# Optimization experiments

Measured on AMD Instinct MI355X. Metric: run time of the kernel, lower is better.

The kernel has to match this reference:

```python
import jax, jax.numpy as jnp
import numpy as np

HIDDEN = 1280
NUM_HEADS = 20
HEAD_DIM = HIDDEN // NUM_HEADS
B, S = 2, 2048


def setup_inputs() -> dict:
    key = jax.random.key(0)
    k1, k2, k3, k4, k5 = jax.random.split(key, 5)
    scale_in = 1.0 / np.sqrt(HIDDEN)
    return {
        "x": jax.random.normal(k1, (B, S, HIDDEN), dtype=jnp.float32),
        "w_attn": jax.random.normal(k2, (HIDDEN, 3 * HIDDEN), dtype=jnp.float32) * scale_in,
        "b_attn": jax.random.normal(k3, (3 * HIDDEN,), dtype=jnp.float32) * 0.02,
        "w_proj": jax.random.normal(k4, (HIDDEN, HIDDEN), dtype=jnp.float32) * scale_in,
        "b_proj": jax.random.normal(k5, (HIDDEN,), dtype=jnp.float32) * 0.02,
    }


def reference(x, w_attn, b_attn, w_proj, b_proj):
    b, s, _ = x.shape
    scale = 1.0 / np.sqrt(HEAD_DIM)
    qkv = x @ w_attn + b_attn                      # [B,S,3H]
    q, k, v = jnp.split(qkv, 3, axis=-1)

    def heads(t):  # [B,S,H] -> [B,nh,S,hd]
        return t.reshape(b, s, NUM_HEADS, HEAD_DIM).transpose(0, 2, 1, 3)

    q, k, v = heads(q), heads(k), heads(v)
    attn = jnp.einsum("bhqd,bhkd->bhqk", q, k) * scale
    causal = jnp.tril(jnp.ones((s, s), dtype=bool))
    attn = jnp.where(causal, attn, jnp.float32(-jnp.inf))
    attn = jax.nn.softmax(attn, axis=-1)           # dropout = identity (eval)
    out = jnp.einsum("bhqk,bhkd->bhqd", attn, v)
    out = out.transpose(0, 2, 1, 3).reshape(b, s, HIDDEN)
    return out @ w_proj + b_proj
```

## Files before the change

kernel.cpp:

```cpp
#include <hip/hip_runtime.h>

typedef unsigned short u16;
typedef __attribute__((ext_vector_type(8))) short bf16x8;
typedef __attribute__((ext_vector_type(4))) float f32x4;
typedef __attribute__((ext_vector_type(4))) unsigned short u16x4;

#define MFMA16 __builtin_amdgcn_mfma_f32_16x16x32_bf16

__device__ __forceinline__ u16 f2bf(float f) {
  unsigned int u = __float_as_uint(f);
  u += 0x7fff + ((u >> 16) & 1);
  return (u16)(u >> 16);
}

__device__ __forceinline__ float vexp2(float x) {
  float r; asm("v_exp_f32 %0, %1" : "=v"(r) : "v"(x)); return r;
}

template<int CTRL>
__device__ __forceinline__ float dppf(float v) {
  return __int_as_float(__builtin_amdgcn_update_dpp(0, __float_as_int(v), CTRL, 0xF, 0xF, true));
}
__device__ __forceinline__ float rowmax16(float v) {
  v = fmaxf(v, dppf<0xB1>(v));
  v = fmaxf(v, dppf<0x4E>(v));
  v = fmaxf(v, dppf<0x141>(v));
  v = fmaxf(v, dppf<0x140>(v));
  return v;
}
__device__ __forceinline__ float rowsum16(float v) {
  v += dppf<0xB1>(v);
  v += dppf<0x4E>(v);
  v += dppf<0x141>(v);
  v += dppf<0x140>(v);
  return v;
}

__device__ __forceinline__ void gload_lds16(const void* g, void* l) {
  __builtin_amdgcn_global_load_lds((__attribute__((address_space(1))) void*)g,
                                   (__attribute__((address_space(3))) void*)l,
                                   16, 0, 0);
}

__global__ void k_cast(const float* __restrict__ src, u16* __restrict__ dst, int n4) {
  int i = blockIdx.x * 256 + threadIdx.x;
  if (i >= n4) return;
  const float4 v = reinterpret_cast<const float4*>(src)[i];
  u16x4 o = {f2bf(v.x), f2bf(v.y), f2bf(v.z), f2bf(v.w)};
  reinterpret_cast<u16x4*>(dst)[i] = o;
}

__global__ void k_transpose_cast(const float* __restrict__ src, u16* __restrict__ dst,
                                 int R, int C) {
  __shared__ float tile[64][65];
  const int t = threadIdx.x;
  const int c0 = blockIdx.x * 64, r0 = blockIdx.y * 64;
#pragma unroll
  for (int i = 0; i < 16; ++i) {
    int e = i * 256 + t;
    int r = e >> 6, c = e & 63;
    tile[r][c] = src[(size_t)(r0 + r) * C + (c0 + c)];
  }
  __syncthreads();
#pragma unroll
  for (int i = 0; i < 16; ++i) {
    int e = i * 256 + t;
    int r = e >> 6, c = e & 63;
    dst[(size_t)(c0 + r) * R + (r0 + c)] = f2bf(tile[c][r]);
  }
}

__global__ void k_transpose_v(const u16* __restrict__ v, u16* __restrict__ vt) {
  __shared__ unsigned int tile[64][65];
  const int t = threadIdx.x;
  const int sblk = blockIdx.x, bh = blockIdx.y;
  {
    const int sl = t >> 2, d0 = (t & 3) * 16;
    const u16* src = v + ((size_t)(bh * 2048 + sblk * 64 + sl) * 64 + d0);
    bf16x8 a = *(const bf16x8*)src;
    bf16x8 b = *(const bf16x8*)(src + 8);
#pragma unroll
    for (int i = 0; i < 8; ++i) {
      tile[sl][d0 + i] = (u16)a[i];
      tile[sl][d0 + 8 + i] = (u16)b[i];
    }
  }
  __syncthreads();
  {
    const int d = t >> 2, s0 = (t & 3) * 16;
    bf16x8 o0, o1;
#pragma unroll
    for (int i = 0; i < 8; ++i) {
      o0[i] = (short)(u16)tile[s0 + i][d];
      o1[i] = (short)(u16)tile[s0 + 8 + i][d];
    }
    u16* dst = vt + ((size_t)(bh * 64 + d) * 2048 + sblk * 64 + s0);
    *(bf16x8*)dst = o0;
    *(bf16x8*)(dst + 8) = o1;
  }
}

__global__ __launch_bounds__(256, 2) void k_gemm_qkv(
    const u16* __restrict__ A, const u16* __restrict__ Bt,
    const float* __restrict__ bias,
    u16* __restrict__ qo, u16* __restrict__ ko, u16* __restrict__ vo) {
  constexpr int K = 1280;
  __shared__ u16 Alds[128 * 64];
  __shared__ u16 Blds[128 * 64];
  const int t = threadIdx.x;
  const int lane = t & 63, wave = t >> 6;
  const int wr = wave >> 1, wc = wave & 1;
  const int l15 = lane & 15, lhi = lane >> 4;
  const int m0 = blockIdx.x * 128, n0 = blockIdx.y * 128;

  f32x4 acc[4][4];
#pragma unroll
  for (int mi = 0; mi < 4; ++mi)
#pragma unroll
    for (int ni = 0; ni < 4; ++ni) acc[mi][ni] = f32x4{0.f, 0.f, 0.f, 0.f};

  const int srow = t >> 3;
  const int scol = (t & 7) * 8;
  const u16* Ag = A + (size_t)(m0 + srow) * K + scol;
  const u16* Bg = Bt + (size_t)(n0 + srow) * K + scol;
  char* Al = (char*)Alds + wave * 1024;
  char* Bl = (char*)Blds + wave * 1024;

  for (int k0 = 0; k0 < K; k0 += 64) {
    __syncthreads();
#pragma unroll
    for (int it = 0; it < 4; ++it) {
      gload_lds16(Ag + (it * 32) * K + k0, Al + it * 4096);
      gload_lds16(Bg + (it * 32) * K + k0, Bl + it * 4096);
    }
    asm volatile("s_waitcnt vmcnt(0)" ::: "memory");
    __syncthreads();
    const u16* Ab = Alds + (wr * 64 + l15) * 64 + lhi * 8;
    const u16* Bb = Blds + (wc * 64 + l15) * 64 + lhi * 8;
    bf16x8 af[4][2], bfv[4][2];
#pragma unroll
    for (int x = 0; x < 4; ++x) {
      af[x][0] = *(const bf16x8*)(Ab + x * 1024);
      af[x][1] = *(const bf16x8*)(Ab + x * 1024 + 32);
      bfv[x][0] = *(const bf16x8*)(Bb + x * 1024);
      bfv[x][1] = *(const bf16x8*)(Bb + x * 1024 + 32);
    }
#pragma unroll
    for (int mi = 0; mi < 4; ++mi)
#pragma unroll
      for (int ni = 0; ni < 4; ++ni) {
        acc[mi][ni] = MFMA16(af[mi][0], bfv[ni][0], acc[mi][ni], 0, 0, 0);
        acc[mi][ni] = MFMA16(af[mi][1], bfv[ni][1], acc[mi][ni], 0, 0, 0);
      }
  }

  const int which = n0 >= 2560 ? 2 : (n0 >= 1280 ? 1 : 0);
  u16* outp = which == 0 ? qo : (which == 1 ? ko : vo);
#pragma unroll
  for (int ni = 0; ni < 4; ++ni) {
    const int n_abs = n0 + wc * 64 + ni * 16 + l15;
    const int nn = n_abs - which * 1280;
    const int h = nn >> 6, d = nn & 63;
    const float bv = bias[n_abs];
#pragma unroll
    for (int mi = 0; mi < 4; ++mi) {
#pragma unroll
      for (int i = 0; i < 4; ++i) {
        const int m_abs = m0 + wr * 64 + mi * 16 + lhi * 4 + i;
        const int bb = m_abs >> 11, ss = m_abs & 2047;
        outp[(((size_t)(bb * 20 + h) * 2048 + ss) << 6) + d] = f2bf(acc[mi][ni][i] + bv);
      }
    }
  }
}

__global__ __launch_bounds__(256, 2) void k_gemm_proj(
    const u16* __restrict__ A, const u16* __restrict__ Bt,
    const float* __restrict__ bias, float* __restrict__ out) {
  constexpr int K = 1280;
  __shared__ u16 Alds[128 * 64];
  __shared__ u16 Blds[128 * 64];
  const int t = threadIdx.x;
  const int lane = t & 63, wave = t >> 6;
  const int wr = wave >> 1, wc = wave & 1;
  const int l15 = lane & 15, lhi = lane >> 4;
  const int m0 = blockIdx.x * 128, n0 = blockIdx.y * 128;

  f32x4 acc[4][4];
#pragma unroll
  for (int mi = 0; mi < 4; ++mi)
#pragma unroll
    for (int ni = 0; ni < 4; ++ni) acc[mi][ni] = f32x4{0.f, 0.f, 0.f, 0.f};

  const int srow = t >> 3;
  const int scol = (t & 7) * 8;
  const u16* Ag = A + (size_t)(m0 + srow) * K + scol;
  const u16* Bg = Bt + (size_t)(n0 + srow) * K + scol;
  char* Al = (char*)Alds + wave * 1024;
  char* Bl = (char*)Blds + wave * 1024;

  for (int k0 = 0; k0 < K; k0 += 64) {
    __syncthreads();
#pragma unroll
    for (int it = 0; it < 4; ++it) {
      gload_lds16(Ag + (it * 32) * K + k0, Al + it * 4096);
      gload_lds16(Bg + (it * 32) * K + k0, Bl + it * 4096);
    }
    asm volatile("s_waitcnt vmcnt(0)" ::: "memory");
    __syncthreads();
    const u16* Ab = Alds + (wr * 64 + l15) * 64 + lhi * 8;
    const u16* Bb = Blds + (wc * 64 + l15) * 64 + lhi * 8;
    bf16x8 af[4][2], bfv[4][2];
#pragma unroll
    for (int x = 0; x < 4; ++x) {
      af[x][0] = *(const bf16x8*)(Ab + x * 1024);
      af[x][1] = *(const bf16x8*)(Ab + x * 1024 + 32);
      bfv[x][0] = *(const bf16x8*)(Bb + x * 1024);
      bfv[x][1] = *(const bf16x8*)(Bb + x * 1024 + 32);
    }
#pragma unroll
    for (int mi = 0; mi < 4; ++mi)
#pragma unroll
      for (int ni = 0; ni < 4; ++ni) {
        acc[mi][ni] = MFMA16(af[mi][0], bfv[ni][0], acc[mi][ni], 0, 0, 0);
        acc[mi][ni] = MFMA16(af[mi][1], bfv[ni][1], acc[mi][ni], 0, 0, 0);
      }
  }

#pragma unroll
  for (int ni = 0; ni < 4; ++ni) {
    const int n_abs = n0 + wc * 64 + ni * 16 + l15;
    const float bv = bias[n_abs];
#pragma unroll
    for (int mi = 0; mi < 4; ++mi) {
#pragma unroll
      for (int i = 0; i < 4; ++i) {
        const int m_abs = m0 + wr * 64 + mi * 16 + lhi * 4 + i;
        out[(size_t)m_abs * 1280 + n_abs] = acc[mi][ni][i] + bv;
      }
    }
  }
}

__global__ __launch_bounds__(256, 3) void k_attn8(
    const u16* __restrict__ Qg, const u16* __restrict__ Kg,
    const u16* __restrict__ VT, u16* __restrict__ ao) {
  __shared__ __align__(16) char kvs[2][16384];
  __shared__ u16 Plds[4][32 * 72];
  const int t = threadIdx.x;
  const int lane = t & 63, wave = t >> 6;
  const int l15 = lane & 15, lhi = lane >> 4;
  const int bh = blockIdx.x;
  const int qt = 15 - blockIdx.y;
  const int bb = bh / 20, hh = bh % 20;
  const int q0w = qt * 128 + wave * 32;
  const int nkv = 2 * (qt + 1);
  const size_t base = (size_t)bh * 2048 * 64;
  const size_t vtb = (size_t)bh * 64 * 2048;
  u16* Pw = Plds[wave];

  const int sls = (lane & 7) ^ (lane >> 3);
  const int soff0 = ((lhi ^ (lane & 7)) << 4);
  const int soff1 = (((4 + lhi) ^ (lane & 7)) << 4);

  bf16x8 qf[2][2];
#pragma unroll
  for (int mr = 0; mr < 2; ++mr)
#pragma unroll
    for (int kk = 0; kk < 2; ++kk)
      qf[mr][kk] = *(const bf16x8*)(Qg + base + (size_t)(q0w + mr * 16 + l15) * 64 + kk * 32 + lhi * 8);

  f32x4 o[2][4];
  float m2[2][4], lp[2][4];
#pragma unroll
  for (int mr = 0; mr < 2; ++mr) {
#pragma unroll
    for (int i = 0; i < 4; ++i) { m2[mr][i] = -3.0e38f; lp[mr][i] = 0.f; }
#pragma unroll
    for (int dc = 0; dc < 4; ++dc) o[mr][dc] = f32x4{0.f, 0.f, 0.f, 0.f};
  }
  const float c1 = 0.18033688f;
  const int lastw = (q0w + 31) >> 6;

  auto stage = [&](char* buf, int kv0) {
#pragma unroll
    for (int j = 0; j < 2; ++j) {
      const int r = j * 32 + wave * 8 + (lane >> 3);
      gload_lds16(Kg + base + (size_t)(kv0 + r) * 64 + sls * 8,
                  buf + j * 4096 + wave * 1024);
      gload_lds16(VT + vtb + (size_t)r * 2048 + kv0 + sls * 8,
                  buf + 8192 + j * 4096 + wave * 1024);
    }
  };

  stage(kvs[0], 0);

  for (int tk = 0; tk < nkv; ++tk) {
    const int kv0 = tk * 64;
    if (tk + 1 < nkv) {
      stage(kvs[(tk + 1) & 1], kv0 + 64);
      asm volatile("s_waitcnt vmcnt(4)" ::: "memory");
    } else {
      asm volatile("s_waitcnt vmcnt(0)" ::: "memory");
    }
    __syncthreads();

    if (tk <= lastw) {
      const char* Kb = kvs[tk & 1];
      const char* Vb = kvs[tk & 1] + 8192;
      const char* Krow = Kb + l15 * 128;
      const char* Vrow = Vb + l15 * 128;
      f32x4 sc[2][4];
#pragma unroll
      for (int c = 0; c < 4; ++c) {
        const bf16x8 kf0 = *(const bf16x8*)(Krow + c * 2048 + soff0);
        const bf16x8 kf1 = *(const bf16x8*)(Krow + c * 2048 + soff1);
#pragma unroll
        for (int mr = 0; mr < 2; ++mr) {
          f32x4 z = (c == 0) ? f32x4{0.f, 0.f, 0.f, 0.f} : sc[mr][c];
          z = MFMA16(qf[mr][0], kf0, f32x4{0.f, 0.f, 0.f, 0.f}, 0, 0, 0);
          z = MFMA16(qf[mr][1], kf1, z, 0, 0, 0);
          sc[mr][c] = z;
        }
      }
      if (kv0 + 63 > q0w) {
#pragma unroll
        for (int mr = 0; mr < 2; ++mr)
#pragma unroll
          for (int c = 0; c < 4; ++c)
#pragma unroll
            for (int i = 0; i < 4; ++i) {
              const int qa = q0w + mr * 16 + lhi * 4 + i;
              const int ka = kv0 + c * 16 + l15;
              sc[mr][c][i] = (ka <= qa) ? sc[mr][c][i] : -3.0e38f;
            }
      }
      float tm[2][4];
      bool need = false;
#pragma unroll
      for (int mr = 0; mr < 2; ++mr)
#pragma unroll
        for (int i = 0; i < 4; ++i) {
          float mx = fmaxf(fmaxf(sc[mr][0][i], sc[mr][1][i]),
                           fmaxf(sc[mr][2][i], sc[mr][3][i]));
          mx = rowmax16(mx) * c1;
          tm[mr][i] = mx;
          need |= (mx > m2[mr][i] + 11.5f);
        }
      if (__any(need)) {
#pragma unroll
        for (int mr = 0; mr < 2; ++mr)
#pragma unroll
          for (int i = 0; i < 4; ++i) {
            const float mn = fmaxf(m2[mr][i], tm[mr][i]);
            const float rs = vexp2(m2[mr][i] - mn);
            m2[mr][i] = mn;
            lp[mr][i] *= rs;
#pragma unroll
            for (int dc = 0; dc < 4; ++dc) o[mr][dc][i] *= rs;
          }
      }
#pragma unroll
      for (int mr = 0; mr < 2; ++mr)
#pragma unroll
        for (int i = 0; i < 4; ++i) {
          float psum = 0.f;
#pragma unroll
          for (int c = 0; c < 4; ++c) {
            const float p = vexp2(__builtin_fmaf(sc[mr][c][i], c1, -m2[mr][i]));
            psum += p;
            Pw[(mr * 16 + lhi * 4 + i) * 72 + c * 16 + l15] = f2bf(p);
          }
          lp[mr][i] += psum;
        }
      bf16x8 pf[2][2];
#pragma unroll
      for (int mr = 0; mr < 2; ++mr)
#pragma unroll
        for (int kk = 0; kk < 2; ++kk)
          pf[mr][kk] = *(const bf16x8*)&Pw[(mr * 16 + l15) * 72 + kk * 32 + lhi * 8];
#pragma unroll
      for (int dc = 0; dc < 4; ++dc) {
        const bf16x8 vf0 = *(const bf16x8*)(Vrow + dc * 2048 + soff0);
        const bf16x8 vf1 = *(const bf16x8*)(Vrow + dc * 2048 + soff1);
#pragma unroll
        for (int mr = 0; mr < 2; ++mr) {
          o[mr][dc] = MFMA16(pf[mr][0], vf0, o[mr][dc], 0, 0, 0);
          o[mr][dc] = MFMA16(pf[mr][1], vf1, o[mr][dc], 0, 0, 0);
        }
      }
    }
    __syncthreads();
  }

#pragma unroll
  for (int mr = 0; mr < 2; ++mr)
#pragma unroll
    for (int i = 0; i < 4; ++i) {
      const float lfull = rowsum16(lp[mr][i]);
      const float inv = 1.0f / lfull;
      const int qa = q0w + mr * 16 + lhi * 4 + i;
#pragma unroll
      for (int dc = 0; dc < 4; ++dc) {
        const int d = dc * 16 + l15;
        ao[((size_t)(bb * 2048 + qa)) * 1280 + hh * 64 + d] = f2bf(o[mr][dc][i] * inv);
      }
    }
}

extern "C" void kernel_launch(void* const* d_in, const int* in_sizes, int n_in,
                              void* d_out, int out_size, void* d_ws, size_t ws_size,
                              hipStream_t stream) {
  (void)in_sizes; (void)n_in; (void)out_size; (void)ws_size;
  const float* x      = (const float*)d_in[0];
  const float* w_attn = (const float*)d_in[1];
  const float* b_attn = (const float*)d_in[2];
  const float* w_proj = (const float*)d_in[3];
  const float* b_proj = (const float*)d_in[4];
  float* out = (float*)d_out;

  char* ws = (char*)d_ws;
  u16* x_bf = (u16*)(ws + 0);
  u16* wa_t = (u16*)(ws + 10485760);
  u16* wp_t = (u16*)(ws + 20316160);
  u16* q_ws = (u16*)(ws + 23592960);
  u16* k_ws = (u16*)(ws + 34078720);
  u16* v_ws = (u16*)(ws + 44564480);
  u16* vt   = x_bf;
  u16* ao   = v_ws;

  k_cast<<<5120, 256, 0, stream>>>(x, x_bf, 4096 * 1280 / 4);
  k_transpose_cast<<<dim3(60, 20), 256, 0, stream>>>(w_attn, wa_t, 1280, 3840);
  k_transpose_cast<<<dim3(20, 20), 256, 0, stream>>>(w_proj, wp_t, 1280, 1280);
  k_gemm_qkv<<<dim3(32, 30), 256, 0, stream>>>(x_bf, wa_t, b_attn, q_ws, k_ws, v_ws);
  k_transpose_v<<<dim3(32, 40), 256, 0, stream>>>(v_ws, vt);
  k_attn8<<<dim3(40, 16), 256, 0, stream>>>(q_ws, k_ws, vt, ao);
  k_gemm_proj<<<dim3(32, 10), 256, 0, stream>>>(ao, wp_t, b_proj, out);
}
```

Baseline: 170.8 us.

## Replace double-buffered LDS K/V with register-staged single buffer, raise occupancy

The attention kernel drops the double-buffered direct global-to-LDS loads. It now uses a single LDS buffer: the next K/V tile is loaded into registers while the current tile is computed, then written to LDS after the barrier. This halves LDS use and raises the launch bounds to four blocks per CU, aiming for more occupancy and latency hiding. It also swaps round-to-nearest bf16 conversion of P for truncation, which is cheaper but slightly less accurate, and removes a dead MFMA-init expression. The costs are extra registers, an extra barrier-to-write dependency per tile, and a small change in numerics.

```diff
diff --git a/kernel.cpp b/kernel.cpp
--- a/kernel.cpp
+++ b/kernel.cpp
@@ -242,10 +242,10 @@
   }
 }
 
-__global__ __launch_bounds__(256, 3) void k_attn8(
+__global__ __launch_bounds__(256, 4) void k_attn9(
     const u16* __restrict__ Qg, const u16* __restrict__ Kg,
     const u16* __restrict__ VT, u16* __restrict__ ao) {
-  __shared__ __align__(16) char kvs[2][16384];
+  __shared__ __align__(16) char kv[16384];
   __shared__ u16 Plds[4][32 * 72];
   const int t = threadIdx.x;
   const int lane = t & 63, wave = t >> 6;
@@ -282,34 +282,36 @@
   const float c1 = 0.18033688f;
   const int lastw = (q0w + 31) >> 6;
 
-  auto stage = [&](char* buf, int kv0) {
+  bf16x8 stgK[2], stgV[2];
+  const int srow0 = wave * 8 + (lane >> 3);
+  auto stage_load = [&](int kv0) {
 #pragma unroll
     for (int j = 0; j < 2; ++j) {
-      const int r = j * 32 + wave * 8 + (lane >> 3);
-      gload_lds16(Kg + base + (size_t)(kv0 + r) * 64 + sls * 8,
-                  buf + j * 4096 + wave * 1024);
-      gload_lds16(VT + vtb + (size_t)r * 2048 + kv0 + sls * 8,
-                  buf + 8192 + j * 4096 + wave * 1024);
+      const int r = j * 32 + srow0;
+      stgK[j] = *(const bf16x8*)(Kg + base + (size_t)(kv0 + r) * 64 + sls * 8);
+      stgV[j] = *(const bf16x8*)(VT + vtb + (size_t)r * 2048 + kv0 + sls * 8);
     }
   };
-
-  stage(kvs[0], 0);
+  auto stage_write = [&]() {
+#pragma unroll
+    for (int j = 0; j < 2; ++j) {
+      *(bf16x8*)(kv + j * 4096 + wave * 1024 + lane * 16) = stgK[j];
+      *(bf16x8*)(kv + 8192 + j * 4096 + wave * 1024 + lane * 16) = stgV[j];
+    }
+  };
+
+  stage_load(0);
+  stage_write();
 
   for (int tk = 0; tk < nkv; ++tk) {
-    const int kv0 = tk * 64;
-    if (tk + 1 < nkv) {
-      stage(kvs[(tk + 1) & 1], kv0 + 64);
-      asm volatile("s_waitcnt vmcnt(4)" ::: "memory");
-    } else {
-      asm volatile("s_waitcnt vmcnt(0)" ::: "memory");
-    }
-    __syncthreads();
+    __syncthreads();
+    const bool more = (tk + 1 < nkv);
+    if (more) stage_load((tk + 1) * 64);
 
     if (tk <= lastw) {
-      const char* Kb = kvs[tk & 1];
-      const char* Vb = kvs[tk & 1] + 8192;
-      const char* Krow = Kb + l15 * 128;
-      const char* Vrow = Vb + l15 * 128;
+      const int kv0 = tk * 64;
+      const char* Krow = kv + l15 * 128;
+      const char* Vrow = kv + 8192 + l15 * 128;
       f32x4 sc[2][4];
 #pragma unroll
       for (int c = 0; c < 4; ++c) {
@@ -317,8 +319,7 @@
         const bf16x8 kf1 = *(const bf16x8*)(Krow + c * 2048 + soff1);
 #pragma unroll
         for (int mr = 0; mr < 2; ++mr) {
-          f32x4 z = (c == 0) ? f32x4{0.f, 0.f, 0.f, 0.f} : sc[mr][c];
-          z = MFMA16(qf[mr][0], kf0, f32x4{0.f, 0.f, 0.f, 0.f}, 0, 0, 0);
+          f32x4 z = MFMA16(qf[mr][0], kf0, f32x4{0.f, 0.f, 0.f, 0.f}, 0, 0, 0);
           z = MFMA16(qf[mr][1], kf1, z, 0, 0, 0);
           sc[mr][c] = z;
         }
@@ -369,7 +370,7 @@
           for (int c = 0; c < 4; ++c) {
             const float p = vexp2(__builtin_fmaf(sc[mr][c][i], c1, -m2[mr][i]));
             psum += p;
-            Pw[(mr * 16 + lhi * 4 + i) * 72 + c * 16 + l15] = f2bf(p);
+            Pw[(mr * 16 + lhi * 4 + i) * 72 + c * 16 + l15] = (u16)(__float_as_uint(p) >> 16);
           }
           lp[mr][i] += psum;
         }
@@ -391,6 +392,7 @@
       }
     }
     __syncthreads();
+    if (more) stage_write();
   }
 
 #pragma unroll
@@ -434,6 +436,6 @@
   k_transpose_cast<<<dim3(20, 20), 256, 0, stream>>>(w_proj, wp_t, 1280, 1280);
   k_gemm_qkv<<<dim3(32, 30), 256, 0, stream>>>(x_bf, wa_t, b_attn, q_ws, k_ws, v_ws);
   k_transpose_v<<<dim3(32, 40), 256, 0, stream>>>(v_ws, vt);
-  k_attn8<<<dim3(40, 16), 256, 0, stream>>>(q_ws, k_ws, vt, ao);
+  k_attn9<<<dim3(40, 16), 256, 0, stream>>>(q_ws, k_ws, vt, ao);
   k_gemm_proj<<<dim3(32, 10), 256, 0, stream>>>(ao, wp_t, b_proj, out);
 }
```

Result: slower. 212.0 us (+24.1%).
